# Performance work log

Hardware: AMD Instinct MI355X
Metric: run time of the kernel (lower is better)

Reference implementation:

```python
import jax, jax.numpy as jnp
import numpy as np

DIM = 1024
HIDDEN = 4096
NUM_EXPERTS = 8
TOP_K = 2
T = 8192


def setup_inputs() -> dict:
    key = jax.random.key(0)
    ks = jax.random.split(key, 5)
    scale = 0.02
    x = jax.random.normal(ks[0], (T, DIM), dtype=jnp.float32)
    gate_w = jax.random.normal(ks[1], (NUM_EXPERTS, DIM), dtype=jnp.float32) * scale  # Linear weight [out,in]
    w1 = jax.random.normal(ks[2], (NUM_EXPERTS, HIDDEN, DIM), dtype=jnp.float32) * scale
    w2 = jax.random.normal(ks[3], (NUM_EXPERTS, DIM, HIDDEN), dtype=jnp.float32) * scale
    w3 = jax.random.normal(ks[4], (NUM_EXPERTS, HIDDEN, DIM), dtype=jnp.float32) * scale
    return {"x": x, "gate_w": gate_w, "w1": w1, "w2": w2, "w3": w3}


def reference(x, gate_w, w1, w2, w3):
    # Router: softmax over all experts, take top-2, renormalize.
    logits = jnp.einsum('td,ed->te', x, gate_w)            # [T, E]
    probs = jax.nn.softmax(logits, axis=-1)
    topw, topi = jax.lax.top_k(probs, TOP_K)               # [T, 2]
    topw = topw / jnp.sum(topw, axis=-1, keepdims=True)
    out = jnp.zeros_like(x)
    num_experts = w1.shape[0]
    for e in range(num_experts):
        # combine weight for expert e per token (0 if not routed here)
        w_e = jnp.sum(jnp.where(topi == e, topw, 0.0), axis=-1)   # [T]
        h = jax.nn.silu(x @ w1[e].T) * (x @ w3[e].T)              # [T, HIDDEN]
        out = out + w_e[:, None] * (h @ w2[e].T)                  # [T, DIM]
    return out
```

## Files before the change

kernel.cpp:

```cpp
#include <hip/hip_runtime.h>
#include <hip/hip_bf16.h>
#include <cstdint>
#include <cstddef>

#define TK 8192
#define DIM 1024
#define HID 4096
#define NE 8

#define SK 32
#define NSUB1 (DIM / SK)
#define NSUB2 (HID / SK)
#define ASZ (512 * 8)
#define BSZ (1024 * 8)

typedef __attribute__((ext_vector_type(8))) __bf16 bfrag;
typedef __attribute__((ext_vector_type(4))) float ffrag;

static __device__ __forceinline__ ushort f2bf(float f) {
    union { float f; uint32_t u; } v; v.f = f;
    uint32_t r = (v.u + 0x7fffu + ((v.u >> 16) & 1u)) >> 16;
    return (ushort)r;
}

static __device__ __forceinline__ uint4 pack8(float4 a, float4 b) {
    union { ushort u[8]; uint4 q; } pk;
    pk.u[0] = f2bf(a.x); pk.u[1] = f2bf(a.y); pk.u[2] = f2bf(a.z); pk.u[3] = f2bf(a.w);
    pk.u[4] = f2bf(b.x); pk.u[5] = f2bf(b.y); pk.u[6] = f2bf(b.z); pk.u[7] = f2bf(b.w);
    return pk.q;
}

static __device__ __forceinline__ void gld16(const ushort* g, ushort* l) {
    __builtin_amdgcn_global_load_lds(
        (const __attribute__((address_space(1))) unsigned int*)g,
        (__attribute__((address_space(3))) unsigned int*)l, 16, 0, 0);
}

#define BARRIER() asm volatile("s_barrier" ::: "memory")
#define WAITVM(N) asm volatile("s_waitcnt vmcnt(" #N ")" ::: "memory")

#define LDSIDX(r, kc) ((((r) >> 3) << 8) + ((kc) << 6) + (((r) & 7) << 3))
#define SLOT_R(s)  ((((s) >> 5) << 3) | ((s) & 7))
#define SLOT_KC(s) (((s) >> 3) & 3)

__global__ __launch_bounds__(256) void k_cvt(const float* __restrict__ src,
                                             ushort* __restrict__ dst, int n8) {
    int i = blockIdx.x * blockDim.x + threadIdx.x;
    if (i >= n8) return;
    const float4* p = (const float4*)src + (size_t)i * 2;
    ((uint4*)dst)[i] = pack8(p[0], p[1]);
}

__global__ __launch_bounds__(256) void k_router(const float* __restrict__ x,
                                                const float* __restrict__ gw,
                                                int* __restrict__ topi, float* __restrict__ topw) {
    int t = blockIdx.x * 4 + (threadIdx.x >> 6);
    int lane = threadIdx.x & 63;
    if (t >= TK) return;
    double acc[NE];
#pragma unroll
    for (int e = 0; e < NE; ++e) acc[e] = 0.0;
    const float* xr = x + (size_t)t * DIM;
    for (int k = lane; k < DIM; k += 64) {
        double xv = (double)xr[k];
#pragma unroll
        for (int e = 0; e < NE; ++e) acc[e] += xv * (double)gw[e * DIM + k];
    }
#pragma unroll
    for (int e = 0; e < NE; ++e) {
#pragma unroll
        for (int off = 32; off > 0; off >>= 1) acc[e] += __shfl_xor(acc[e], off);
    }
    if (lane == 0) {
        int i1 = 0;
#pragma unroll
        for (int e = 1; e < NE; ++e) if (acc[e] > acc[i1]) i1 = e;
        int i2 = (i1 == 0) ? 1 : 0;
#pragma unroll
        for (int e = 0; e < NE; ++e) if (e != i1 && acc[e] > acc[i2]) i2 = e;
        double w = 1.0 / (1.0 + exp(acc[i2] - acc[i1]));
        topi[t * 2 + 0] = i1; topi[t * 2 + 1] = i2;
        topw[t * 2 + 0] = (float)w; topw[t * 2 + 1] = (float)(1.0 - w);
    }
}

__global__ void k_count(const int* __restrict__ topi, int* __restrict__ counts) {
    int i = blockIdx.x * blockDim.x + threadIdx.x;
    if (i < 2 * TK) atomicAdd(&counts[topi[i]], 1);
}

__global__ void k_scan(const int* __restrict__ counts, int* __restrict__ offs,
                       int* __restrict__ cursor, int* __restrict__ desc,
                       int* __restrict__ ndesc) {
    if (threadIdx.x == 0 && blockIdx.x == 0) {
        int s = 0, d = 0;
        for (int e = 0; e < NE; ++e) {
            offs[e] = s; cursor[e] = s;
            int tiles = (counts[e] + 127) >> 7;
            for (int t = 0; t < tiles; ++t) desc[d++] = (e << 16) | t;
            s += counts[e];
        }
        offs[NE] = s;
        ndesc[0] = d;
    }
}

__global__ void k_scatter(const int* __restrict__ topi, const float* __restrict__ topw,
                          int* __restrict__ cursor, int* __restrict__ perm, float* __restrict__ pw) {
    int t = blockIdx.x * blockDim.x + threadIdx.x;
    if (t >= TK) return;
#pragma unroll
    for (int k = 0; k < 2; ++k) {
        int e = topi[t * 2 + k];
        int pos = atomicAdd(&cursor[e], 1);
        perm[pos] = t; pw[pos] = topw[t * 2 + k];
    }
}


__global__ __launch_bounds__(512, 4) void k_ffn1(const ushort* __restrict__ xb,
                                                 const ushort* __restrict__ w1b,
                                                 const ushort* __restrict__ w3b,
                                                 const int* __restrict__ offs,
                                                 const int* __restrict__ perm,
                                                 const int* __restrict__ desc,
                                                 const int* __restrict__ ndesc_g,
                                                 ushort* __restrict__ H) {
    __shared__ ushort lA[3 * ASZ];
    __shared__ ushort lB[3 * BSZ];
    __shared__ int lTok[128];

    const int tid = threadIdx.x;
    const int lane = tid & 63, wid = tid >> 6;
    const int l15 = lane & 15, kcc = lane >> 4;
    const int wm = (wid >> 2) * 64;
    const int wn = (wid & 3) * 64;

    const int nitems = ndesc_g[0] << 5;

    const int rA = SLOT_R(tid), kcA = SLOT_KC(tid);

    bfrag a[4], b[4];
    ffrag acc[4][4];

#pragma unroll 1
    for (int w = blockIdx.x; w < nitems; w += (int)gridDim.x) {
        __syncthreads();
        const int de = desc[w >> 5];
        const int e = de >> 16, mt = de & 0xffff, nt = w & 31;
        const int m0 = offs[e] + (mt << 7);
        const int nrows = min(128, offs[e + 1] - m0);
        if (tid < 128) lTok[tid] = (tid < nrows) ? perm[m0 + tid] : perm[m0];
        __syncthreads();

        const ushort* pA = xb + (size_t)lTok[rA] * DIM + kcA * 8;
        const ushort* pBp[2];
        {
            const size_t ebase = (size_t)e * HID * DIM;
#pragma unroll
            for (int i2 = 0; i2 < 2; ++i2) {
                int s = i2 * 512 + tid;
                int r = SLOT_R(s), kc = SLOT_KC(s);
                int gg = r >> 4;
                int h = ((gg >> 1) << 4) | (r & 15);
                const ushort* wsrc = (gg & 1) ? w3b : w1b;
                pBp[i2] = wsrc + ebase + (size_t)(nt * 128 + h) * DIM + kc * 8;
            }
        }

#pragma unroll
        for (int i = 0; i < 4; ++i)
#pragma unroll
            for (int j = 0; j < 4; ++j) acc[i][j] = (ffrag)0.f;

#define STG1(buf, sx) do { if ((sx) < NSUB1) {                                   \
            gld16(pA + (sx) * SK, lA + (buf) * ASZ + (wid * 64) * 8);            \
            gld16(pBp[0] + (sx) * SK, lB + (buf) * BSZ + (wid * 64) * 8);        \
            gld16(pBp[1] + (sx) * SK, lB + (buf) * BSZ + (512 + wid * 64) * 8); } } while (0)

        STG1(0, 0);
        STG1(1, 1);
        int bc = 0, bs = 2;
#pragma unroll 1
        for (int X = 0; X < NSUB1 - 1; ++X) {
            WAITVM(3);
            BARRIER();
            const ushort* A_ = lA + bc * ASZ;
            const ushort* B_ = lB + bc * BSZ;
#pragma unroll
            for (int j = 0; j < 4; ++j) b[j] = *(const bfrag*)&B_[LDSIDX(wn + j * 16 + l15, kcc)];
#pragma unroll
            for (int i = 0; i < 4; ++i) a[i] = *(const bfrag*)&A_[LDSIDX(wm + i * 16 + l15, kcc)];
            STG1(bs, X + 2);
            __builtin_amdgcn_s_setprio(1);
#pragma unroll
            for (int i = 0; i < 4; ++i)
#pragma unroll
                for (int j = 0; j < 4; ++j)
                    acc[i][j] = __builtin_amdgcn_mfma_f32_16x16x32_bf16(a[i], b[j], acc[i][j], 0, 0, 0);
            __builtin_amdgcn_s_setprio(0);
            bc = (bc == 2) ? 0 : bc + 1;
            bs = (bs == 2) ? 0 : bs + 1;
        }
        {
            WAITVM(0);
            BARRIER();
            const ushort* A_ = lA + bc * ASZ;
            const ushort* B_ = lB + bc * BSZ;
#pragma unroll
            for (int j = 0; j < 4; ++j) b[j] = *(const bfrag*)&B_[LDSIDX(wn + j * 16 + l15, kcc)];
#pragma unroll
            for (int i = 0; i < 4; ++i) a[i] = *(const bfrag*)&A_[LDSIDX(wm + i * 16 + l15, kcc)];
            __builtin_amdgcn_s_setprio(1);
#pragma unroll
            for (int i = 0; i < 4; ++i)
#pragma unroll
                for (int j = 0; j < 4; ++j)
                    acc[i][j] = __builtin_amdgcn_mfma_f32_16x16x32_bf16(a[i], b[j], acc[i][j], 0, 0, 0);
            __builtin_amdgcn_s_setprio(0);
        }
#undef STG1

#pragma unroll
        for (int i = 0; i < 4; ++i) {
            int rbase = wm + i * 16 + ((lane >> 4) << 2);
#pragma unroll
            for (int q = 0; q < 4; ++q) {
                int rl = rbase + q;
                if (rl >= nrows) continue;
                size_t rowoff = (size_t)(m0 + rl) * HID;
#pragma unroll
                for (int jf = 0; jf < 4; jf += 2) {
                    int gg = (wn >> 4) + jf;
                    int col = nt * 128 + ((gg >> 1) << 4) + l15;
                    float h1 = acc[i][jf][q], h3 = acc[i][jf + 1][q];
                    H[rowoff + col] = f2bf((h1 / (1.f + __expf(-h1))) * h3);
                }
            }
        }
    }
}

__global__ __launch_bounds__(512, 4) void k_ffn2(const ushort* __restrict__ H,
                                                 const ushort* __restrict__ w2b,
                                                 const int* __restrict__ offs,
                                                 const int* __restrict__ perm,
                                                 const float* __restrict__ pw,
                                                 const int* __restrict__ desc,
                                                 const int* __restrict__ ndesc_g,
                                                 float* __restrict__ out) {
    __shared__ ushort lA[3 * ASZ];
    __shared__ ushort lB[3 * BSZ];
    __shared__ int lTok[128];
    __shared__ float lPw[128];

    const int tid = threadIdx.x;
    const int lane = tid & 63, wid = tid >> 6;
    const int l15 = lane & 15, kcc = lane >> 4;
    const int wm = (wid >> 2) * 64;
    const int wn = (wid & 3) * 64;

    const int nitems = ndesc_g[0] << 2;

    const int rA = SLOT_R(tid), kcA = SLOT_KC(tid);

    bfrag a[4], b[4];
    ffrag acc[4][4];

#pragma unroll 1
    for (int w = blockIdx.x; w < nitems; w += (int)gridDim.x) {
        __syncthreads();
        const int de = desc[w >> 2];
        const int e = de >> 16, mt = de & 0xffff, nt = w & 3;
        const int m0 = offs[e] + (mt << 7);
        const int nrows = min(128, offs[e + 1] - m0);
        if (tid < 128) {
            bool v = tid < nrows;
            lTok[tid] = v ? perm[m0 + tid] : 0;
            lPw[tid]  = v ? pw[m0 + tid] : 0.f;
        }
        __syncthreads();

        int posA = m0 + rA; if (posA > 2 * TK - 1) posA = 2 * TK - 1;
        const ushort* pA = H + (size_t)posA * HID + kcA * 8;
        const ushort* pBp[2];
        {
            const size_t ebase = (size_t)e * DIM * HID;
#pragma unroll
            for (int i2 = 0; i2 < 2; ++i2) {
                int s = i2 * 512 + tid;
                int r = SLOT_R(s), kc = SLOT_KC(s);
                pBp[i2] = w2b + ebase + (size_t)(nt * 256 + r) * HID + kc * 8;
            }
        }

#pragma unroll
        for (int i = 0; i < 4; ++i)
#pragma unroll
            for (int j = 0; j < 4; ++j) acc[i][j] = (ffrag)0.f;

#define STG2(buf, sx) do { if ((sx) < NSUB2) {                                   \
            gld16(pA + (sx) * SK, lA + (buf) * ASZ + (wid * 64) * 8);            \
            gld16(pBp[0] + (sx) * SK, lB + (buf) * BSZ + (wid * 64) * 8);        \
            gld16(pBp[1] + (sx) * SK, lB + (buf) * BSZ + (512 + wid * 64) * 8); } } while (0)

        STG2(0, 0);
        STG2(1, 1);
        int bc = 0, bs = 2;
#pragma unroll 1
        for (int X = 0; X < NSUB2 - 1; ++X) {
            WAITVM(3);
            BARRIER();
            const ushort* A_ = lA + bc * ASZ;
            const ushort* B_ = lB + bc * BSZ;
#pragma unroll
            for (int j = 0; j < 4; ++j) b[j] = *(const bfrag*)&B_[LDSIDX(wn + j * 16 + l15, kcc)];
#pragma unroll
            for (int i = 0; i < 4; ++i) a[i] = *(const bfrag*)&A_[LDSIDX(wm + i * 16 + l15, kcc)];
            STG2(bs, X + 2);
            __builtin_amdgcn_s_setprio(1);
#pragma unroll
            for (int i = 0; i < 4; ++i)
#pragma unroll
                for (int j = 0; j < 4; ++j)
                    acc[i][j] = __builtin_amdgcn_mfma_f32_16x16x32_bf16(a[i], b[j], acc[i][j], 0, 0, 0);
            __builtin_amdgcn_s_setprio(0);
            bc = (bc == 2) ? 0 : bc + 1;
            bs = (bs == 2) ? 0 : bs + 1;
        }
        {
            WAITVM(0);
            BARRIER();
            const ushort* A_ = lA + bc * ASZ;
            const ushort* B_ = lB + bc * BSZ;
#pragma unroll
            for (int j = 0; j < 4; ++j) b[j] = *(const bfrag*)&B_[LDSIDX(wn + j * 16 + l15, kcc)];
#pragma unroll
            for (int i = 0; i < 4; ++i) a[i] = *(const bfrag*)&A_[LDSIDX(wm + i * 16 + l15, kcc)];
            __builtin_amdgcn_s_setprio(1);
#pragma unroll
            for (int i = 0; i < 4; ++i)
#pragma unroll
                for (int j = 0; j < 4; ++j)
                    acc[i][j] = __builtin_amdgcn_mfma_f32_16x16x32_bf16(a[i], b[j], acc[i][j], 0, 0, 0);
            __builtin_amdgcn_s_setprio(0);
        }
#undef STG2

#pragma unroll
        for (int i = 0; i < 4; ++i) {
            int rbase = wm + i * 16 + ((lane >> 4) << 2);
#pragma unroll
            for (int q = 0; q < 4; ++q) {
                int rl = rbase + q;
                if (rl >= nrows) continue;
                int tok = lTok[rl];
                float wgt = lPw[rl];
                size_t rowoff = (size_t)tok * DIM;
#pragma unroll
                for (int j = 0; j < 4; ++j) {
                    int col = nt * 256 + wn + j * 16 + l15;
                    atomicAdd(&out[rowoff + col], acc[i][j][q] * wgt);
                }
            }
        }
    }
}

extern "C" void kernel_launch(void* const* d_in, const int* in_sizes, int n_in,
                              void* d_out, int out_size, void* d_ws, size_t ws_size,
                              hipStream_t stream) {
    const float* x  = (const float*)d_in[0];
    const float* gw = (const float*)d_in[1];
    const float* w1 = (const float*)d_in[2];
    const float* w2 = (const float*)d_in[3];
    const float* w3 = (const float*)d_in[4];
    float* out = (float*)d_out;

    char* ws = (char*)d_ws;
    int*    topi   = (int*)(ws + 0);
    float*  topw   = (float*)(ws + 65536);
    int*    perm   = (int*)(ws + 131072);
    float*  pw     = (float*)(ws + 196608);
    int*    counts = (int*)(ws + 262144);
    int*    offs   = (int*)(ws + 262144 + 256);
    int*    cursor = (int*)(ws + 262144 + 512);
    int*    ndesc  = (int*)(ws + 262144 + 768);
    int*    desc   = (int*)(ws + 262144 + 1024);

    const size_t OFF_XB = 524288;
    const size_t OFF_H  = OFF_XB + 16777216;
    const size_t OFF_WA = OFF_H + 134217728;
    const size_t OFF_WB = OFF_WA + 67108864;

    ushort* xb  = (ushort*)(ws + OFF_XB);
    ushort* H   = (ushort*)(ws + OFF_H);
    ushort* wA  = (ushort*)(ws + OFF_WA);
    ushort* wB  = (ushort*)(ws + OFF_WB);

    hipMemsetAsync(counts, 0, 32, stream);
    hipMemsetAsync(out, 0, (size_t)out_size * sizeof(float), stream);

    k_router<<<dim3(TK / 4), 256, 0, stream>>>(x, gw, topi, topw);
    k_count<<<dim3((2 * TK) / 256), 256, 0, stream>>>(topi, counts);
    k_scan<<<dim3(1), 64, 0, stream>>>(counts, offs, cursor, desc, ndesc);
    k_scatter<<<dim3(TK / 256), 256, 0, stream>>>(topi, topw, cursor, perm, pw);

    k_cvt<<<dim3((TK * DIM / 8) / 256), 256, 0, stream>>>(x, xb, TK * DIM / 8);
    k_cvt<<<dim3((NE * HID * DIM / 8) / 256), 256, 0, stream>>>(w1, wA, NE * HID * DIM / 8);
    k_cvt<<<dim3((NE * HID * DIM / 8) / 256), 256, 0, stream>>>(w3, wB, NE * HID * DIM / 8);

    k_ffn1<<<dim3(512), 512, 0, stream>>>(xb, wA, wB, offs, perm, desc, ndesc, H);

    k_cvt<<<dim3((NE * DIM * HID / 8) / 256), 256, 0, stream>>>(w2, wA, NE * DIM * HID / 8);

    k_ffn2<<<dim3(512), 512, 0, stream>>>(H, wA, offs, perm, pw, desc, ndesc, out);
}
```

Baseline: 1.003 ms.

## Pre-swizzle weights into MFMA fragment layout and load B directly to registers

Weights are now converted into a fragment-major bf16 layout (w1/w3 interleaved, and w2 likewise), so each wave loads its B operands straight from global memory into registers with coalesced 16-byte loads instead of staging them through LDS. Only the gathered token rows (A) still go through LDS, now with a 4-stage buffer. Blocks shrink to 256 threads with 128x128 tiles and twice the grid, which frees LDS and should raise occupancy. The cost is B tiles being reloaded per wave with no LDS sharing, so global/L2 traffic goes up, and register-level B loads have to hide their own latency.

```diff
diff --git a/kernel.cpp b/kernel.cpp
--- a/kernel.cpp
+++ b/kernel.cpp
@@ -11,8 +11,7 @@
 #define SK 32
 #define NSUB1 (DIM / SK)
 #define NSUB2 (HID / SK)
-#define ASZ (512 * 8)
-#define BSZ (1024 * 8)
+#define ASZ 4096
 
 typedef __attribute__((ext_vector_type(8))) __bf16 bfrag;
 typedef __attribute__((ext_vector_type(4))) float ffrag;
@@ -49,6 +48,30 @@
     if (i >= n8) return;
     const float4* p = (const float4*)src + (size_t)i * 2;
     ((uint4*)dst)[i] = pack8(p[0], p[1]);
+}
+
+__global__ __launch_bounds__(256) void k_cvt_w13t(const float* __restrict__ w1,
+                                                  const float* __restrict__ w3,
+                                                  ushort* __restrict__ dst) {
+    int i = blockIdx.x * blockDim.x + threadIdx.x;
+    int cc = i & 63, kb = (i >> 6) & 31, g = i >> 11;
+    int e = g >> 9, nt = (g >> 3) & 63, gg = g & 7;
+    int row15 = cc & 15, kc = cc >> 4;
+    int h = nt * 64 + (((gg >> 1) << 4) | row15);
+    const float* src = (gg & 1) ? w3 : w1;
+    const float* p = src + ((size_t)e * HID + h) * DIM + kb * 32 + kc * 8;
+    ((uint4*)dst)[i] = pack8(*(const float4*)p, *(const float4*)(p + 4));
+}
+
+__global__ __launch_bounds__(256) void k_cvt_w2t(const float* __restrict__ w2,
+                                                 ushort* __restrict__ dst) {
+    int i = blockIdx.x * blockDim.x + threadIdx.x;
+    int cc = i & 63, kb = (i >> 6) & 127, g = i >> 13;
+    int e = g >> 6, nt = (g >> 3) & 7, g2 = g & 7;
+    int row15 = cc & 15, kc = cc >> 4;
+    int row = nt * 128 + g2 * 16 + row15;
+    const float* p = w2 + ((size_t)e * DIM + row) * HID + kb * 32 + kc * 8;
+    ((uint4*)dst)[i] = pack8(*(const float4*)p, *(const float4*)(p + 4));
 }
 
 __global__ __launch_bounds__(256) void k_router(const float* __restrict__ x,
@@ -118,108 +141,86 @@
 }
 
 
-__global__ __launch_bounds__(512, 4) void k_ffn1(const ushort* __restrict__ xb,
-                                                 const ushort* __restrict__ w1b,
-                                                 const ushort* __restrict__ w3b,
+__global__ __launch_bounds__(256, 4) void k_ffn1(const ushort* __restrict__ xb,
+                                                 const ushort* __restrict__ w13t,
                                                  const int* __restrict__ offs,
                                                  const int* __restrict__ perm,
                                                  const int* __restrict__ desc,
                                                  const int* __restrict__ ndesc_g,
                                                  ushort* __restrict__ H) {
-    __shared__ ushort lA[3 * ASZ];
-    __shared__ ushort lB[3 * BSZ];
+    __shared__ ushort lA[4 * ASZ];
     __shared__ int lTok[128];
 
     const int tid = threadIdx.x;
     const int lane = tid & 63, wid = tid >> 6;
     const int l15 = lane & 15, kcc = lane >> 4;
-    const int wm = (wid >> 2) * 64;
-    const int wn = (wid & 3) * 64;
-
-    const int nitems = ndesc_g[0] << 5;
-
-    const int rA = SLOT_R(tid), kcA = SLOT_KC(tid);
-
-    bfrag a[4], b[4];
+    const int wm = (wid >> 1) * 64;
+    const int wn = (wid & 1) * 64;
+    const int gbase = wn >> 4;
+
+    const int rA0 = SLOT_R(tid), kA0 = SLOT_KC(tid);
+    const int rA1 = SLOT_R(tid + 256), kA1 = SLOT_KC(tid + 256);
+
+    const int nitems = ndesc_g[0] << 6;
+
+    bfrag a[4], br[4];
     ffrag acc[4][4];
 
 #pragma unroll 1
     for (int w = blockIdx.x; w < nitems; w += (int)gridDim.x) {
         __syncthreads();
-        const int de = desc[w >> 5];
-        const int e = de >> 16, mt = de & 0xffff, nt = w & 31;
+        const int de = desc[w >> 6];
+        const int e = de >> 16, mt = de & 0xffff, nt = w & 63;
         const int m0 = offs[e] + (mt << 7);
         const int nrows = min(128, offs[e + 1] - m0);
         if (tid < 128) lTok[tid] = (tid < nrows) ? perm[m0 + tid] : perm[m0];
         __syncthreads();
 
-        const ushort* pA = xb + (size_t)lTok[rA] * DIM + kcA * 8;
-        const ushort* pBp[2];
-        {
-            const size_t ebase = (size_t)e * HID * DIM;
-#pragma unroll
-            for (int i2 = 0; i2 < 2; ++i2) {
-                int s = i2 * 512 + tid;
-                int r = SLOT_R(s), kc = SLOT_KC(s);
-                int gg = r >> 4;
-                int h = ((gg >> 1) << 4) | (r & 15);
-                const ushort* wsrc = (gg & 1) ? w3b : w1b;
-                pBp[i2] = wsrc + ebase + (size_t)(nt * 128 + h) * DIM + kc * 8;
-            }
-        }
+        const ushort* pA0 = xb + (size_t)lTok[rA0] * DIM + kA0 * 8;
+        const ushort* pA1 = xb + (size_t)lTok[rA1] * DIM + kA1 * 8;
+        const ushort* pBw = w13t + ((size_t)(e * 512 + nt * 8 + gbase) << 14) + lane * 8;
 
 #pragma unroll
         for (int i = 0; i < 4; ++i)
 #pragma unroll
             for (int j = 0; j < 4; ++j) acc[i][j] = (ffrag)0.f;
 
-#define STG1(buf, sx) do { if ((sx) < NSUB1) {                                   \
-            gld16(pA + (sx) * SK, lA + (buf) * ASZ + (wid * 64) * 8);            \
-            gld16(pBp[0] + (sx) * SK, lB + (buf) * BSZ + (wid * 64) * 8);        \
-            gld16(pBp[1] + (sx) * SK, lB + (buf) * BSZ + (512 + wid * 64) * 8); } } while (0)
-
-        STG1(0, 0);
-        STG1(1, 1);
-        int bc = 0, bs = 2;
+#define STGA1(buf, sx) do { \
+            gld16(pA0 + (sx) * SK, lA + (buf) * ASZ + wid * 512); \
+            gld16(pA1 + (sx) * SK, lA + (buf) * ASZ + 2048 + wid * 512); } while (0)
+#define LOADB1(kb) { _Pragma("unroll") \
+            for (int j = 0; j < 4; ++j) \
+                br[j] = *(const bfrag*)(pBw + ((size_t)j << 14) + (size_t)(kb) * 512); }
+#define ITER1(X, BR, BW) do { \
+            if ((X) == NSUB1 - 1) { WAITVM(0); } else { WAITVM(2); } \
+            BARRIER(); \
+            _Pragma("unroll") \
+            for (int i = 0; i < 4; ++i) \
+                a[i] = *(const bfrag*)&lA[(BR) * ASZ + LDSIDX(wm + i * 16 + l15, kcc)]; \
+            __builtin_amdgcn_s_setprio(1); \
+            _Pragma("unroll") \
+            for (int i = 0; i < 4; ++i) \
+                _Pragma("unroll") \
+                for (int j = 0; j < 4; ++j) \
+                    acc[i][j] = __builtin_amdgcn_mfma_f32_16x16x32_bf16(a[i], br[j], acc[i][j], 0, 0, 0); \
+            __builtin_amdgcn_s_setprio(0); \
+            if ((X) + 1 < NSUB1) LOADB1((X) + 1); \
+            if ((X) + 2 < NSUB1) STGA1(BW, (X) + 2); \
+        } while (0)
+
+        STGA1(0, 0);
+        LOADB1(0);
+        STGA1(1, 1);
 #pragma unroll 1
-        for (int X = 0; X < NSUB1 - 1; ++X) {
-            WAITVM(3);
-            BARRIER();
-            const ushort* A_ = lA + bc * ASZ;
-            const ushort* B_ = lB + bc * BSZ;
-#pragma unroll
-            for (int j = 0; j < 4; ++j) b[j] = *(const bfrag*)&B_[LDSIDX(wn + j * 16 + l15, kcc)];
-#pragma unroll
-            for (int i = 0; i < 4; ++i) a[i] = *(const bfrag*)&A_[LDSIDX(wm + i * 16 + l15, kcc)];
-            STG1(bs, X + 2);
-            __builtin_amdgcn_s_setprio(1);
-#pragma unroll
-            for (int i = 0; i < 4; ++i)
-#pragma unroll
-                for (int j = 0; j < 4; ++j)
-                    acc[i][j] = __builtin_amdgcn_mfma_f32_16x16x32_bf16(a[i], b[j], acc[i][j], 0, 0, 0);
-            __builtin_amdgcn_s_setprio(0);
-            bc = (bc == 2) ? 0 : bc + 1;
-            bs = (bs == 2) ? 0 : bs + 1;
-        }
-        {
-            WAITVM(0);
-            BARRIER();
-            const ushort* A_ = lA + bc * ASZ;
-            const ushort* B_ = lB + bc * BSZ;
-#pragma unroll
-            for (int j = 0; j < 4; ++j) b[j] = *(const bfrag*)&B_[LDSIDX(wn + j * 16 + l15, kcc)];
-#pragma unroll
-            for (int i = 0; i < 4; ++i) a[i] = *(const bfrag*)&A_[LDSIDX(wm + i * 16 + l15, kcc)];
-            __builtin_amdgcn_s_setprio(1);
-#pragma unroll
-            for (int i = 0; i < 4; ++i)
-#pragma unroll
-                for (int j = 0; j < 4; ++j)
-                    acc[i][j] = __builtin_amdgcn_mfma_f32_16x16x32_bf16(a[i], b[j], acc[i][j], 0, 0, 0);
-            __builtin_amdgcn_s_setprio(0);
-        }
-#undef STG1
+        for (int X4 = 0; X4 < NSUB1; X4 += 4) {
+            ITER1(X4 + 0, 0, 2);
+            ITER1(X4 + 1, 1, 3);
+            ITER1(X4 + 2, 2, 0);
+            ITER1(X4 + 3, 3, 1);
+        }
+#undef ITER1
+#undef LOADB1
+#undef STGA1
 
 #pragma unroll
         for (int i = 0; i < 4; ++i) {
@@ -231,8 +232,8 @@
                 size_t rowoff = (size_t)(m0 + rl) * HID;
 #pragma unroll
                 for (int jf = 0; jf < 4; jf += 2) {
-                    int gg = (wn >> 4) + jf;
-                    int col = nt * 128 + ((gg >> 1) << 4) + l15;
+                    int gg = gbase + jf;
+                    int col = nt * 64 + ((gg >> 1) << 4) + l15;
                     float h1 = acc[i][jf][q], h3 = acc[i][jf + 1][q];
                     H[rowoff + col] = f2bf((h1 / (1.f + __expf(-h1))) * h3);
                 }
@@ -241,37 +242,38 @@
     }
 }
 
-__global__ __launch_bounds__(512, 4) void k_ffn2(const ushort* __restrict__ H,
-                                                 const ushort* __restrict__ w2b,
+__global__ __launch_bounds__(256, 4) void k_ffn2(const ushort* __restrict__ H,
+                                                 const ushort* __restrict__ w2t,
                                                  const int* __restrict__ offs,
                                                  const int* __restrict__ perm,
                                                  const float* __restrict__ pw,
                                                  const int* __restrict__ desc,
                                                  const int* __restrict__ ndesc_g,
                                                  float* __restrict__ out) {
-    __shared__ ushort lA[3 * ASZ];
-    __shared__ ushort lB[3 * BSZ];
+    __shared__ ushort lA[4 * ASZ];
     __shared__ int lTok[128];
     __shared__ float lPw[128];
 
     const int tid = threadIdx.x;
     const int lane = tid & 63, wid = tid >> 6;
     const int l15 = lane & 15, kcc = lane >> 4;
-    const int wm = (wid >> 2) * 64;
-    const int wn = (wid & 3) * 64;
-
-    const int nitems = ndesc_g[0] << 2;
-
-    const int rA = SLOT_R(tid), kcA = SLOT_KC(tid);
-
-    bfrag a[4], b[4];
+    const int wm = (wid >> 1) * 64;
+    const int wn = (wid & 1) * 64;
+    const int gbase = wn >> 4;
+
+    const int rA0 = SLOT_R(tid), kA0 = SLOT_KC(tid);
+    const int rA1 = SLOT_R(tid + 256), kA1 = SLOT_KC(tid + 256);
+
+    const int nitems = ndesc_g[0] << 3;
+
+    bfrag a[4], br[4];
     ffrag acc[4][4];
 
 #pragma unroll 1
     for (int w = blockIdx.x; w < nitems; w += (int)gridDim.x) {
         __syncthreads();
-        const int de = desc[w >> 2];
-        const int e = de >> 16, mt = de & 0xffff, nt = w & 3;
+        const int de = desc[w >> 3];
+        const int e = de >> 16, mt = de & 0xffff, nt = w & 7;
         const int m0 = offs[e] + (mt << 7);
         const int nrows = min(128, offs[e + 1] - m0);
         if (tid < 128) {
@@ -281,71 +283,53 @@
         }
         __syncthreads();
 
-        int posA = m0 + rA; if (posA > 2 * TK - 1) posA = 2 * TK - 1;
-        const ushort* pA = H + (size_t)posA * HID + kcA * 8;
-        const ushort* pBp[2];
-        {
-            const size_t ebase = (size_t)e * DIM * HID;
-#pragma unroll
-            for (int i2 = 0; i2 < 2; ++i2) {
-                int s = i2 * 512 + tid;
-                int r = SLOT_R(s), kc = SLOT_KC(s);
-                pBp[i2] = w2b + ebase + (size_t)(nt * 256 + r) * HID + kc * 8;
-            }
-        }
+        int p0 = m0 + rA0; if (p0 > 2 * TK - 1) p0 = 2 * TK - 1;
+        int p1 = m0 + rA1; if (p1 > 2 * TK - 1) p1 = 2 * TK - 1;
+        const ushort* pA0 = H + (size_t)p0 * HID + kA0 * 8;
+        const ushort* pA1 = H + (size_t)p1 * HID + kA1 * 8;
+        const ushort* pBw = w2t + ((size_t)(e * 64 + nt * 8 + gbase) << 16) + lane * 8;
 
 #pragma unroll
         for (int i = 0; i < 4; ++i)
 #pragma unroll
             for (int j = 0; j < 4; ++j) acc[i][j] = (ffrag)0.f;
 
-#define STG2(buf, sx) do { if ((sx) < NSUB2) {                                   \
-            gld16(pA + (sx) * SK, lA + (buf) * ASZ + (wid * 64) * 8);            \
-            gld16(pBp[0] + (sx) * SK, lB + (buf) * BSZ + (wid * 64) * 8);        \
-            gld16(pBp[1] + (sx) * SK, lB + (buf) * BSZ + (512 + wid * 64) * 8); } } while (0)
-
-        STG2(0, 0);
-        STG2(1, 1);
-        int bc = 0, bs = 2;
+#define STGA2(buf, sx) do { \
+            gld16(pA0 + (sx) * SK, lA + (buf) * ASZ + wid * 512); \
+            gld16(pA1 + (sx) * SK, lA + (buf) * ASZ + 2048 + wid * 512); } while (0)
+#define LOADB2(kb) { _Pragma("unroll") \
+            for (int j = 0; j < 4; ++j) \
+                br[j] = *(const bfrag*)(pBw + ((size_t)j << 16) + (size_t)(kb) * 512); }
+#define ITER2(X, BR, BW) do { \
+            if ((X) == NSUB2 - 1) { WAITVM(0); } else { WAITVM(2); } \
+            BARRIER(); \
+            _Pragma("unroll") \
+            for (int i = 0; i < 4; ++i) \
+                a[i] = *(const bfrag*)&lA[(BR) * ASZ + LDSIDX(wm + i * 16 + l15, kcc)]; \
+            __builtin_amdgcn_s_setprio(1); \
+            _Pragma("unroll") \
+            for (int i = 0; i < 4; ++i) \
+                _Pragma("unroll") \
+                for (int j = 0; j < 4; ++j) \
+                    acc[i][j] = __builtin_amdgcn_mfma_f32_16x16x32_bf16(a[i], br[j], acc[i][j], 0, 0, 0); \
+            __builtin_amdgcn_s_setprio(0); \
+            if ((X) + 1 < NSUB2) LOADB2((X) + 1); \
+            if ((X) + 2 < NSUB2) STGA2(BW, (X) + 2); \
+        } while (0)
+
+        STGA2(0, 0);
+        LOADB2(0);
+        STGA2(1, 1);
 #pragma unroll 1
-        for (int X = 0; X < NSUB2 - 1; ++X) {
-            WAITVM(3);
-            BARRIER();
-            const ushort* A_ = lA + bc * ASZ;
-            const ushort* B_ = lB + bc * BSZ;
-#pragma unroll
-            for (int j = 0; j < 4; ++j) b[j] = *(const bfrag*)&B_[LDSIDX(wn + j * 16 + l15, kcc)];
-#pragma unroll
-            for (int i = 0; i < 4; ++i) a[i] = *(const bfrag*)&A_[LDSIDX(wm + i * 16 + l15, kcc)];
-            STG2(bs, X + 2);
-            __builtin_amdgcn_s_setprio(1);
-#pragma unroll
-            for (int i = 0; i < 4; ++i)
-#pragma unroll
-                for (int j = 0; j < 4; ++j)
-                    acc[i][j] = __builtin_amdgcn_mfma_f32_16x16x32_bf16(a[i], b[j], acc[i][j], 0, 0, 0);
-            __builtin_amdgcn_s_setprio(0);
-            bc = (bc == 2) ? 0 : bc + 1;
-            bs = (bs == 2) ? 0 : bs + 1;
-        }
-        {
-            WAITVM(0);
-            BARRIER();
-            const ushort* A_ = lA + bc * ASZ;
-            const ushort* B_ = lB + bc * BSZ;
-#pragma unroll
-            for (int j = 0; j < 4; ++j) b[j] = *(const bfrag*)&B_[LDSIDX(wn + j * 16 + l15, kcc)];
-#pragma unroll
-            for (int i = 0; i < 4; ++i) a[i] = *(const bfrag*)&A_[LDSIDX(wm + i * 16 + l15, kcc)];
-            __builtin_amdgcn_s_setprio(1);
-#pragma unroll
-            for (int i = 0; i < 4; ++i)
-#pragma unroll
-                for (int j = 0; j < 4; ++j)
-                    acc[i][j] = __builtin_amdgcn_mfma_f32_16x16x32_bf16(a[i], b[j], acc[i][j], 0, 0, 0);
-            __builtin_amdgcn_s_setprio(0);
-        }
-#undef STG2
+        for (int X4 = 0; X4 < NSUB2; X4 += 4) {
+            ITER2(X4 + 0, 0, 2);
+            ITER2(X4 + 1, 1, 3);
+            ITER2(X4 + 2, 2, 0);
+            ITER2(X4 + 3, 3, 1);
+        }
+#undef ITER2
+#undef LOADB2
+#undef STGA2
 
 #pragma unroll
         for (int i = 0; i < 4; ++i) {
@@ -359,7 +343,7 @@
                 size_t rowoff = (size_t)tok * DIM;
 #pragma unroll
                 for (int j = 0; j < 4; ++j) {
-                    int col = nt * 256 + wn + j * 16 + l15;
+                    int col = nt * 128 + wn + j * 16 + l15;
                     atomicAdd(&out[rowoff + col], acc[i][j][q] * wgt);
                 }
             }
@@ -390,13 +374,12 @@
 
     const size_t OFF_XB = 524288;
     const size_t OFF_H  = OFF_XB + 16777216;
-    const size_t OFF_WA = OFF_H + 134217728;
-    const size_t OFF_WB = OFF_WA + 67108864;
-
-    ushort* xb  = (ushort*)(ws + OFF_XB);
-    ushort* H   = (ushort*)(ws + OFF_H);
-    ushort* wA  = (ushort*)(ws + OFF_WA);
-    ushort* wB  = (ushort*)(ws + OFF_WB);
+    const size_t OFF_WT = OFF_H + 134217728;
+
+    ushort* xb   = (ushort*)(ws + OFF_XB);
+    ushort* H    = (ushort*)(ws + OFF_H);
+    ushort* w13t = (ushort*)(ws + OFF_WT);
+    ushort* w2t  = (ushort*)(ws + OFF_WT);
 
     hipMemsetAsync(counts, 0, 32, stream);
     hipMemsetAsync(out, 0, (size_t)out_size * sizeof(float), stream);
@@ -407,12 +390,11 @@
     k_scatter<<<dim3(TK / 256), 256, 0, stream>>>(topi, topw, cursor, perm, pw);
 
     k_cvt<<<dim3((TK * DIM / 8) / 256), 256, 0, stream>>>(x, xb, TK * DIM / 8);
-    k_cvt<<<dim3((NE * HID * DIM / 8) / 256), 256, 0, stream>>>(w1, wA, NE * HID * DIM / 8);
-    k_cvt<<<dim3((NE * HID * DIM / 8) / 256), 256, 0, stream>>>(w3, wB, NE * HID * DIM / 8);
-
-    k_ffn1<<<dim3(512), 512, 0, stream>>>(xb, wA, wB, offs, perm, desc, ndesc, H);
-
-    k_cvt<<<dim3((NE * DIM * HID / 8) / 256), 256, 0, stream>>>(w2, wA, NE * DIM * HID / 8);
-
-    k_ffn2<<<dim3(512), 512, 0, stream>>>(H, wA, offs, perm, pw, desc, ndesc, out);
-}
+    k_cvt_w13t<<<dim3(32768), 256, 0, stream>>>(w1, w3, w13t);
+
+    k_ffn1<<<dim3(1024), 256, 0, stream>>>(xb, w13t, offs, perm, desc, ndesc, H);
+
+    k_cvt_w2t<<<dim3(16384), 256, 0, stream>>>(w2, w2t);
+
+    k_ffn2<<<dim3(1024), 256, 0, stream>>>(H, w2t, offs, perm, pw, desc, ndesc, out);
+}
```

Result: slower. 1.475 ms (+47.2%).

## Use 4-wave blocks with 128x64 per-wave tiles in both FFN GEMMs

Applied to the files above, without the earlier changes.

Both expert FFN kernels switch from 8 waves of 64x64 tiles to 4 waves that each cover all 128 rows and 64 columns. Each wave loads its B fragments once and reuses them across two A halves, so each thread issues twice as many global-to-LDS copies per stage. The goal is less LDS read traffic per MFMA and fewer waves contending at barriers. The cost is doubled accumulator registers (8x4 fragments), launch bounds lowered to 256 threads with 2 blocks, and fewer waves available to hide latency.

```diff
diff --git a/kernel.cpp b/kernel.cpp
--- a/kernel.cpp
+++ b/kernel.cpp
@@ -11,8 +11,8 @@
 #define SK 32
 #define NSUB1 (DIM / SK)
 #define NSUB2 (HID / SK)
-#define ASZ (512 * 8)
-#define BSZ (1024 * 8)
+#define ASZ 4096
+#define BSZ 8192
 
 typedef __attribute__((ext_vector_type(8))) __bf16 bfrag;
 typedef __attribute__((ext_vector_type(4))) float ffrag;
@@ -118,7 +118,7 @@
 }
 
 
-__global__ __launch_bounds__(512, 4) void k_ffn1(const ushort* __restrict__ xb,
+__global__ __launch_bounds__(256, 2) void k_ffn1(const ushort* __restrict__ xb,
                                                  const ushort* __restrict__ w1b,
                                                  const ushort* __restrict__ w3b,
                                                  const int* __restrict__ offs,
@@ -133,15 +133,16 @@
     const int tid = threadIdx.x;
     const int lane = tid & 63, wid = tid >> 6;
     const int l15 = lane & 15, kcc = lane >> 4;
-    const int wm = (wid >> 2) * 64;
-    const int wn = (wid & 3) * 64;
+    const int wn = wid * 64;
+    const int gbase = wn >> 4;
 
     const int nitems = ndesc_g[0] << 5;
 
-    const int rA = SLOT_R(tid), kcA = SLOT_KC(tid);
+    const int rA0 = SLOT_R(tid), kA0 = SLOT_KC(tid);
+    const int rA1 = SLOT_R(tid + 256), kA1 = SLOT_KC(tid + 256);
 
     bfrag a[4], b[4];
-    ffrag acc[4][4];
+    ffrag acc[8][4];
 
 #pragma unroll 1
     for (int w = blockIdx.x; w < nitems; w += (int)gridDim.x) {
@@ -153,44 +154,47 @@
         if (tid < 128) lTok[tid] = (tid < nrows) ? perm[m0 + tid] : perm[m0];
         __syncthreads();
 
-        const ushort* pA = xb + (size_t)lTok[rA] * DIM + kcA * 8;
-        const ushort* pBp[2];
+        const ushort* pA0 = xb + (size_t)lTok[rA0] * DIM + kA0 * 8;
+        const ushort* pA1 = xb + (size_t)lTok[rA1] * DIM + kA1 * 8;
+        const ushort* pB[4];
         {
             const size_t ebase = (size_t)e * HID * DIM;
 #pragma unroll
-            for (int i2 = 0; i2 < 2; ++i2) {
-                int s = i2 * 512 + tid;
+            for (int c = 0; c < 4; ++c) {
+                int s = c * 256 + tid;
                 int r = SLOT_R(s), kc = SLOT_KC(s);
                 int gg = r >> 4;
                 int h = ((gg >> 1) << 4) | (r & 15);
                 const ushort* wsrc = (gg & 1) ? w3b : w1b;
-                pBp[i2] = wsrc + ebase + (size_t)(nt * 128 + h) * DIM + kc * 8;
+                pB[c] = wsrc + ebase + (size_t)(nt * 128 + h) * DIM + kc * 8;
             }
         }
 
 #pragma unroll
-        for (int i = 0; i < 4; ++i)
+        for (int i = 0; i < 8; ++i)
 #pragma unroll
             for (int j = 0; j < 4; ++j) acc[i][j] = (ffrag)0.f;
 
-#define STG1(buf, sx) do { if ((sx) < NSUB1) {                                   \
-            gld16(pA + (sx) * SK, lA + (buf) * ASZ + (wid * 64) * 8);            \
-            gld16(pBp[0] + (sx) * SK, lB + (buf) * BSZ + (wid * 64) * 8);        \
-            gld16(pBp[1] + (sx) * SK, lB + (buf) * BSZ + (512 + wid * 64) * 8); } } while (0)
-
-        STG1(0, 0);
-        STG1(1, 1);
+#define STG1(buf, sx) do { if ((sx) < NSUB1) {                                    \
+            gld16(pA0 + (sx) * SK, lA + (buf) * ASZ + (wid * 64) * 8);            \
+            gld16(pA1 + (sx) * SK, lA + (buf) * ASZ + (256 + wid * 64) * 8);      \
+            gld16(pB[0] + (sx) * SK, lB + (buf) * BSZ + (wid * 64) * 8);          \
+            gld16(pB[1] + (sx) * SK, lB + (buf) * BSZ + (256 + wid * 64) * 8);    \
+            gld16(pB[2] + (sx) * SK, lB + (buf) * BSZ + (512 + wid * 64) * 8);    \
+            gld16(pB[3] + (sx) * SK, lB + (buf) * BSZ + (768 + wid * 64) * 8); } } while (0)
+
+        STG1(0, 0); STG1(1, 1);
         int bc = 0, bs = 2;
 #pragma unroll 1
-        for (int X = 0; X < NSUB1 - 1; ++X) {
-            WAITVM(3);
+        for (int X = 0; X < NSUB1; ++X) {
+            if (X < NSUB1 - 1) { WAITVM(6); } else { WAITVM(0); }
             BARRIER();
             const ushort* A_ = lA + bc * ASZ;
             const ushort* B_ = lB + bc * BSZ;
 #pragma unroll
             for (int j = 0; j < 4; ++j) b[j] = *(const bfrag*)&B_[LDSIDX(wn + j * 16 + l15, kcc)];
 #pragma unroll
-            for (int i = 0; i < 4; ++i) a[i] = *(const bfrag*)&A_[LDSIDX(wm + i * 16 + l15, kcc)];
+            for (int i = 0; i < 4; ++i) a[i] = *(const bfrag*)&A_[LDSIDX(i * 16 + l15, kcc)];
             STG1(bs, X + 2);
             __builtin_amdgcn_s_setprio(1);
 #pragma unroll
@@ -199,31 +203,23 @@
                 for (int j = 0; j < 4; ++j)
                     acc[i][j] = __builtin_amdgcn_mfma_f32_16x16x32_bf16(a[i], b[j], acc[i][j], 0, 0, 0);
             __builtin_amdgcn_s_setprio(0);
+#pragma unroll
+            for (int i = 0; i < 4; ++i) a[i] = *(const bfrag*)&A_[LDSIDX(64 + i * 16 + l15, kcc)];
+            __builtin_amdgcn_s_setprio(1);
+#pragma unroll
+            for (int i = 0; i < 4; ++i)
+#pragma unroll
+                for (int j = 0; j < 4; ++j)
+                    acc[4 + i][j] = __builtin_amdgcn_mfma_f32_16x16x32_bf16(a[i], b[j], acc[4 + i][j], 0, 0, 0);
+            __builtin_amdgcn_s_setprio(0);
             bc = (bc == 2) ? 0 : bc + 1;
             bs = (bs == 2) ? 0 : bs + 1;
         }
-        {
-            WAITVM(0);
-            BARRIER();
-            const ushort* A_ = lA + bc * ASZ;
-            const ushort* B_ = lB + bc * BSZ;
-#pragma unroll
-            for (int j = 0; j < 4; ++j) b[j] = *(const bfrag*)&B_[LDSIDX(wn + j * 16 + l15, kcc)];
-#pragma unroll
-            for (int i = 0; i < 4; ++i) a[i] = *(const bfrag*)&A_[LDSIDX(wm + i * 16 + l15, kcc)];
-            __builtin_amdgcn_s_setprio(1);
-#pragma unroll
-            for (int i = 0; i < 4; ++i)
-#pragma unroll
-                for (int j = 0; j < 4; ++j)
-                    acc[i][j] = __builtin_amdgcn_mfma_f32_16x16x32_bf16(a[i], b[j], acc[i][j], 0, 0, 0);
-            __builtin_amdgcn_s_setprio(0);
-        }
 #undef STG1
 
 #pragma unroll
-        for (int i = 0; i < 4; ++i) {
-            int rbase = wm + i * 16 + ((lane >> 4) << 2);
+        for (int i = 0; i < 8; ++i) {
+            int rbase = i * 16 + ((lane >> 4) << 2);
 #pragma unroll
             for (int q = 0; q < 4; ++q) {
                 int rl = rbase + q;
@@ -231,7 +227,7 @@
                 size_t rowoff = (size_t)(m0 + rl) * HID;
 #pragma unroll
                 for (int jf = 0; jf < 4; jf += 2) {
-                    int gg = (wn >> 4) + jf;
+                    int gg = gbase + jf;
                     int col = nt * 128 + ((gg >> 1) << 4) + l15;
                     float h1 = acc[i][jf][q], h3 = acc[i][jf + 1][q];
                     H[rowoff + col] = f2bf((h1 / (1.f + __expf(-h1))) * h3);
@@ -241,7 +237,7 @@
     }
 }
 
-__global__ __launch_bounds__(512, 4) void k_ffn2(const ushort* __restrict__ H,
+__global__ __launch_bounds__(256, 2) void k_ffn2(const ushort* __restrict__ H,
                                                  const ushort* __restrict__ w2b,
                                                  const int* __restrict__ offs,
                                                  const int* __restrict__ perm,
@@ -257,15 +253,15 @@
     const int tid = threadIdx.x;
     const int lane = tid & 63, wid = tid >> 6;
     const int l15 = lane & 15, kcc = lane >> 4;
-    const int wm = (wid >> 2) * 64;
-    const int wn = (wid & 3) * 64;
+    const int wn = wid * 64;
 
     const int nitems = ndesc_g[0] << 2;
 
-    const int rA = SLOT_R(tid), kcA = SLOT_KC(tid);
+    const int rA0 = SLOT_R(tid), kA0 = SLOT_KC(tid);
+    const int rA1 = SLOT_R(tid + 256), kA1 = SLOT_KC(tid + 256);
 
     bfrag a[4], b[4];
-    ffrag acc[4][4];
+    ffrag acc[8][4];
 
 #pragma unroll 1
     for (int w = blockIdx.x; w < nitems; w += (int)gridDim.x) {
@@ -281,42 +277,46 @@
         }
         __syncthreads();
 
-        int posA = m0 + rA; if (posA > 2 * TK - 1) posA = 2 * TK - 1;
-        const ushort* pA = H + (size_t)posA * HID + kcA * 8;
-        const ushort* pBp[2];
+        int p0 = m0 + rA0; if (p0 > 2 * TK - 1) p0 = 2 * TK - 1;
+        int p1 = m0 + rA1; if (p1 > 2 * TK - 1) p1 = 2 * TK - 1;
+        const ushort* pA0 = H + (size_t)p0 * HID + kA0 * 8;
+        const ushort* pA1 = H + (size_t)p1 * HID + kA1 * 8;
+        const ushort* pB[4];
         {
             const size_t ebase = (size_t)e * DIM * HID;
 #pragma unroll
-            for (int i2 = 0; i2 < 2; ++i2) {
-                int s = i2 * 512 + tid;
+            for (int c = 0; c < 4; ++c) {
+                int s = c * 256 + tid;
                 int r = SLOT_R(s), kc = SLOT_KC(s);
-                pBp[i2] = w2b + ebase + (size_t)(nt * 256 + r) * HID + kc * 8;
+                pB[c] = w2b + ebase + (size_t)(nt * 256 + r) * HID + kc * 8;
             }
         }
 
 #pragma unroll
-        for (int i = 0; i < 4; ++i)
+        for (int i = 0; i < 8; ++i)
 #pragma unroll
             for (int j = 0; j < 4; ++j) acc[i][j] = (ffrag)0.f;
 
-#define STG2(buf, sx) do { if ((sx) < NSUB2) {                                   \
-            gld16(pA + (sx) * SK, lA + (buf) * ASZ + (wid * 64) * 8);            \
-            gld16(pBp[0] + (sx) * SK, lB + (buf) * BSZ + (wid * 64) * 8);        \
-            gld16(pBp[1] + (sx) * SK, lB + (buf) * BSZ + (512 + wid * 64) * 8); } } while (0)
-
-        STG2(0, 0);
-        STG2(1, 1);
+#define STG2(buf, sx) do { if ((sx) < NSUB2) {                                    \
+            gld16(pA0 + (sx) * SK, lA + (buf) * ASZ + (wid * 64) * 8);            \
+            gld16(pA1 + (sx) * SK, lA + (buf) * ASZ + (256 + wid * 64) * 8);      \
+            gld16(pB[0] + (sx) * SK, lB + (buf) * BSZ + (wid * 64) * 8);          \
+            gld16(pB[1] + (sx) * SK, lB + (buf) * BSZ + (256 + wid * 64) * 8);    \
+            gld16(pB[2] + (sx) * SK, lB + (buf) * BSZ + (512 + wid * 64) * 8);    \
+            gld16(pB[3] + (sx) * SK, lB + (buf) * BSZ + (768 + wid * 64) * 8); } } while (0)
+
+        STG2(0, 0); STG2(1, 1);
         int bc = 0, bs = 2;
 #pragma unroll 1
-        for (int X = 0; X < NSUB2 - 1; ++X) {
-            WAITVM(3);
+        for (int X = 0; X < NSUB2; ++X) {
+            if (X < NSUB2 - 1) { WAITVM(6); } else { WAITVM(0); }
             BARRIER();
             const ushort* A_ = lA + bc * ASZ;
             const ushort* B_ = lB + bc * BSZ;
 #pragma unroll
             for (int j = 0; j < 4; ++j) b[j] = *(const bfrag*)&B_[LDSIDX(wn + j * 16 + l15, kcc)];
 #pragma unroll
-            for (int i = 0; i < 4; ++i) a[i] = *(const bfrag*)&A_[LDSIDX(wm + i * 16 + l15, kcc)];
+            for (int i = 0; i < 4; ++i) a[i] = *(const bfrag*)&A_[LDSIDX(i * 16 + l15, kcc)];
             STG2(bs, X + 2);
             __builtin_amdgcn_s_setprio(1);
 #pragma unroll
@@ -325,31 +325,23 @@
                 for (int j = 0; j < 4; ++j)
                     acc[i][j] = __builtin_amdgcn_mfma_f32_16x16x32_bf16(a[i], b[j], acc[i][j], 0, 0, 0);
             __builtin_amdgcn_s_setprio(0);
+#pragma unroll
+            for (int i = 0; i < 4; ++i) a[i] = *(const bfrag*)&A_[LDSIDX(64 + i * 16 + l15, kcc)];
+            __builtin_amdgcn_s_setprio(1);
+#pragma unroll
+            for (int i = 0; i < 4; ++i)
+#pragma unroll
+                for (int j = 0; j < 4; ++j)
+                    acc[4 + i][j] = __builtin_amdgcn_mfma_f32_16x16x32_bf16(a[i], b[j], acc[4 + i][j], 0, 0, 0);
+            __builtin_amdgcn_s_setprio(0);
             bc = (bc == 2) ? 0 : bc + 1;
             bs = (bs == 2) ? 0 : bs + 1;
         }
-        {
-            WAITVM(0);
-            BARRIER();
-            const ushort* A_ = lA + bc * ASZ;
-            const ushort* B_ = lB + bc * BSZ;
-#pragma unroll
-            for (int j = 0; j < 4; ++j) b[j] = *(const bfrag*)&B_[LDSIDX(wn + j * 16 + l15, kcc)];
-#pragma unroll
-            for (int i = 0; i < 4; ++i) a[i] = *(const bfrag*)&A_[LDSIDX(wm + i * 16 + l15, kcc)];
-            __builtin_amdgcn_s_setprio(1);
-#pragma unroll
-            for (int i = 0; i < 4; ++i)
-#pragma unroll
-                for (int j = 0; j < 4; ++j)
-                    acc[i][j] = __builtin_amdgcn_mfma_f32_16x16x32_bf16(a[i], b[j], acc[i][j], 0, 0, 0);
-            __builtin_amdgcn_s_setprio(0);
-        }
 #undef STG2
 
 #pragma unroll
-        for (int i = 0; i < 4; ++i) {
-            int rbase = wm + i * 16 + ((lane >> 4) << 2);
+        for (int i = 0; i < 8; ++i) {
+            int rbase = i * 16 + ((lane >> 4) << 2);
 #pragma unroll
             for (int q = 0; q < 4; ++q) {
                 int rl = rbase + q;
@@ -410,9 +402,9 @@
     k_cvt<<<dim3((NE * HID * DIM / 8) / 256), 256, 0, stream>>>(w1, wA, NE * HID * DIM / 8);
     k_cvt<<<dim3((NE * HID * DIM / 8) / 256), 256, 0, stream>>>(w3, wB, NE * HID * DIM / 8);
 
-    k_ffn1<<<dim3(512), 512, 0, stream>>>(xb, wA, wB, offs, perm, desc, ndesc, H);
+    k_ffn1<<<dim3(512), 256, 0, stream>>>(xb, wA, wB, offs, perm, desc, ndesc, H);
 
     k_cvt<<<dim3((NE * DIM * HID / 8) / 256), 256, 0, stream>>>(w2, wA, NE * DIM * HID / 8);
 
-    k_ffn2<<<dim3(512), 512, 0, stream>>>(H, wA, offs, perm, pw, desc, ndesc, out);
-}
+    k_ffn2<<<dim3(512), 256, 0, stream>>>(H, wA, offs, perm, pw, desc, ndesc, out);
+}
```

New measurement: 1.092 ms. 1.09x slower.
